# Optimization experiments

Measured on AMD Instinct MI355X. Metric: run time of the kernel, lower is better.

Reference implementation:

```python
import jax, jax.numpy as jnp
import numpy as np


def setup_inputs() -> dict:
    key = jax.random.key(0)
    k1, k2 = jax.random.split(key)
    enc = jax.random.normal(k1, (32, 64, 64, 64), dtype=jnp.float32)   # (B, C, H, W), C == D
    embed = jax.random.normal(k2, (512, 64), dtype=jnp.float32)        # (K, D) codebook
    return {"enc": enc, "embed": embed}


def reference(enc, embed):
    B, C, H, W = enc.shape
    K, D = embed.shape
    # torch: enc.view(B, -1, C) with C == D -> plain reshape (no transpose), faithful to source.
    x = enc.reshape(B, -1, D)                                          # (B, N, D), N = C*H*W/D
    # Squared L2 distances; argmin is invariant under sqrt so we skip torch.cdist's sqrt.
    x_sq = jnp.sum(x * x, axis=-1, keepdims=True)                      # (B, N, 1)
    e_sq = jnp.sum(embed * embed, axis=-1)                             # (K,)
    d2 = x_sq - 2.0 * jnp.einsum('bnd,kd->bnk', x, embed) + e_sq       # (B, N, K)
    closest = jnp.argmin(d2, axis=-1)                                  # (B, N) int
    quantized = embed[closest]                                         # (B, N, D) gather
    commitment_loss = jnp.mean((jax.lax.stop_gradient(quantized) - x) ** 2)
    codebook_loss = jnp.mean((quantized - jax.lax.stop_gradient(x)) ** 2)
    quantize_loss = codebook_loss + 1.0 * commitment_loss
    # Straight-through estimator.
    quant_out = (x + jax.lax.stop_gradient(quantized - x)).reshape(B, C, H, W)
    return quant_out, quantize_loss, closest
```

## Files before the change

kernel.cpp:

```cpp
#include <hip/hip_runtime.h>
#include <math.h>

#define DQ 64
#define KQ 512
#define NVEC 131072
#define QOUT_SIZE (NVEC * DQ)
#define LOSS_OFF QOUT_SIZE
#define IDX_OFF (QOUT_SIZE + 1)

#define RPW 32
#define WPB 4
#define VPB (RPW * WPB)
#define NBLK (NVEC / VPB)
#define SC 64
#define NST (KQ / SC)
#define SDQ (SC * DQ)
#define TIE_THR 0.01f

typedef __attribute__((ext_vector_type(8))) short short8;
typedef __attribute__((ext_vector_type(4))) float f32x4;

static __device__ __forceinline__ unsigned short f2bf(float f) {
    unsigned u = __float_as_uint(f);
    u += 0x7fff + ((u >> 16) & 1);
    return (unsigned short)(u >> 16);
}
static __device__ __forceinline__ float bf2f(unsigned short h) {
    return __uint_as_float(((unsigned)h) << 16);
}
static __device__ __forceinline__ void cvt8(float4 a, float4 b, short8& hi, short8& lo) {
#define C1(I, V) { unsigned short _h = f2bf(V); hi[I] = (short)_h; lo[I] = (short)f2bf((V) - bf2f(_h)); }
    C1(0, a.x) C1(1, a.y) C1(2, a.z) C1(3, a.w)
    C1(4, b.x) C1(5, b.y) C1(6, b.z) C1(7, b.w)
#undef C1
}

__global__ void vq_init_kernel(const float* __restrict__ embed,
                               unsigned short* __restrict__ ehi,
                               unsigned short* __restrict__ elo,
                               float* __restrict__ esq,
                               float* __restrict__ out) {
    const int t = blockIdx.x * 64 + threadIdx.x;
    if (t == 0) out[LOSS_OFF] = 0.0f;
    const int k = t >> 3;
    const int c = t & 7;
    const float4* p = (const float4*)(embed + (size_t)k * DQ + c * 8);
    float4 a = p[0], b = p[1];
    short8 hi, lo;
    cvt8(a, b, hi, lo);
    const int slot = c ^ (k & 7);
    *(short8*)(ehi + (size_t)k * DQ + slot * 8) = hi;
    *(short8*)(elo + (size_t)k * DQ + slot * 8) = lo;

    float ps = 0.f;
    ps = fmaf(a.x, a.x, ps); ps = fmaf(a.y, a.y, ps); ps = fmaf(a.z, a.z, ps); ps = fmaf(a.w, a.w, ps);
    ps = fmaf(b.x, b.x, ps); ps = fmaf(b.y, b.y, ps); ps = fmaf(b.z, b.z, ps); ps = fmaf(b.w, b.w, ps);
    ps += __shfl_xor(ps, 1);
    ps += __shfl_xor(ps, 2);
    ps += __shfl_xor(ps, 4);
    if (c == 0) esq[k] = ps;
}

__global__ __launch_bounds__(256) void vq_mfma_kernel(const float* __restrict__ enc,
                                                      const float* __restrict__ embed,
                                                      const unsigned short* __restrict__ ehi,
                                                      const unsigned short* __restrict__ elo,
                                                      const float* __restrict__ esq,
                                                      float* __restrict__ out) {
    __shared__ unsigned short hs[2 * SDQ];
    __shared__ unsigned short ls_[2 * SDQ];
    __shared__ float esq_s[KQ];
    __shared__ int bidx_s[VPB];
    __shared__ int flag_s[VPB];
    __shared__ float red[WPB];

    const int tid = threadIdx.x;
    const int lane = tid & 63;
    const int w = tid >> 6;
    const int l15 = lane & 15;
    const int l4 = lane >> 4;
    const int vb = blockIdx.x * VPB + w * RPW;

    esq_s[tid] = esq[tid];
    esq_s[tid + 256] = esq[tid + 256];

    short8 ahA[2], alA[2], ahB[2], alB[2];
#pragma unroll
    for (int a = 0; a < 2; a++) {
        const float* base = enc + (size_t)(vb + a * 16 + l15) * DQ + l4 * 8;
        const float4* p0 = (const float4*)base;
        const float4* p1 = (const float4*)(base + 32);
        cvt8(p0[0], p0[1], ahA[a], alA[a]);
        cvt8(p1[0], p1[1], ahB[a], alB[a]);
    }

    float m1[8], m2[8];
    int i1[8];
#pragma unroll
    for (int r = 0; r < 8; r++) { m1[r] = 3.4e38f; m2[r] = 3.4e38f; i1[r] = 0; }

    const int sl0 = (l4 ^ (l15 & 7)) * 8;
    const int sl1 = sl0 ^ 32;

    short8 rh0 = *(const short8*)(ehi + tid * 8);
    short8 rh1 = *(const short8*)(ehi + 2048 + tid * 8);
    short8 rl0 = *(const short8*)(elo + tid * 8);
    short8 rl1 = *(const short8*)(elo + 2048 + tid * 8);
    *(short8*)(hs + tid * 8) = rh0;  *(short8*)(hs + 2048 + tid * 8) = rh1;
    *(short8*)(ls_ + tid * 8) = rl0; *(short8*)(ls_ + 2048 + tid * 8) = rl1;
    rh0 = *(const short8*)(ehi + SDQ + tid * 8);
    rh1 = *(const short8*)(ehi + SDQ + 2048 + tid * 8);
    rl0 = *(const short8*)(elo + SDQ + tid * 8);
    rl1 = *(const short8*)(elo + SDQ + 2048 + tid * 8);

#define LDB(H0, H1, L0, L1, S) { const int _o = ((S) * 16 + l15) * DQ; \
    H0 = *(const short8*)(hb + _o + sl0); H1 = *(const short8*)(hb + _o + sl1); \
    L0 = *(const short8*)(lb + _o + sl0); L1 = *(const short8*)(lb + _o + sl1); }

#define BODY(ST, S, BH0, BH1, BL0, BL1) { \
    const int code = (ST) * SC + (S) * 16 + l15; \
    const float ev = esq_s[code]; \
    _Pragma("unroll") \
    for (int a = 0; a < 2; a++) { \
        f32x4 acc = {0.f, 0.f, 0.f, 0.f}; \
        acc = __builtin_amdgcn_mfma_f32_16x16x32_bf16(ahA[a], BH0, acc, 0, 0, 0); \
        acc = __builtin_amdgcn_mfma_f32_16x16x32_bf16(ahB[a], BH1, acc, 0, 0, 0); \
        acc = __builtin_amdgcn_mfma_f32_16x16x32_bf16(alA[a], BH0, acc, 0, 0, 0); \
        acc = __builtin_amdgcn_mfma_f32_16x16x32_bf16(alB[a], BH1, acc, 0, 0, 0); \
        acc = __builtin_amdgcn_mfma_f32_16x16x32_bf16(ahA[a], BL0, acc, 0, 0, 0); \
        acc = __builtin_amdgcn_mfma_f32_16x16x32_bf16(ahB[a], BL1, acc, 0, 0, 0); \
        _Pragma("unroll") \
        for (int r = 0; r < 4; r++) { \
            float v = fmaf(-2.0f, acc[r], ev); \
            bool lt = v < m1[a * 4 + r]; \
            i1[a * 4 + r] = lt ? code : i1[a * 4 + r]; \
            m2[a * 4 + r] = fminf(m2[a * 4 + r], fmaxf(m1[a * 4 + r], v)); \
            m1[a * 4 + r] = fminf(m1[a * 4 + r], v); \
        } \
    } }

    for (int st = 0; st < NST; st++) {
        __syncthreads();
        if (st < NST - 1) {
            unsigned short* hw = hs + ((st + 1) & 1) * SDQ;
            unsigned short* lw = ls_ + ((st + 1) & 1) * SDQ;
            *(short8*)(hw + tid * 8) = rh0;  *(short8*)(hw + 2048 + tid * 8) = rh1;
            *(short8*)(lw + tid * 8) = rl0;  *(short8*)(lw + 2048 + tid * 8) = rl1;
        }
        if (st < NST - 2) {
            const int o = (st + 2) * SDQ;
            rh0 = *(const short8*)(ehi + o + tid * 8);
            rh1 = *(const short8*)(ehi + o + 2048 + tid * 8);
            rl0 = *(const short8*)(elo + o + tid * 8);
            rl1 = *(const short8*)(elo + o + 2048 + tid * 8);
        }
        const unsigned short* hb = hs + (st & 1) * SDQ;
        const unsigned short* lb = ls_ + (st & 1) * SDQ;
        short8 b0h0, b0h1, b0l0, b0l1, b1h0, b1h1, b1l0, b1l1;
        LDB(b0h0, b0h1, b0l0, b0l1, 0)
        LDB(b1h0, b1h1, b1l0, b1l1, 1)
        BODY(st, 0, b0h0, b0h1, b0l0, b0l1)
        LDB(b0h0, b0h1, b0l0, b0l1, 2)
        BODY(st, 1, b1h0, b1h1, b1l0, b1l1)
        LDB(b1h0, b1h1, b1l0, b1l1, 3)
        BODY(st, 2, b0h0, b0h1, b0l0, b0l1)
        BODY(st, 3, b1h0, b1h1, b1l0, b1l1)
    }
#undef LDB
#undef BODY

#pragma unroll
    for (int m = 1; m <= 8; m <<= 1) {
#pragma unroll
        for (int r = 0; r < 8; r++) {
            float o1 = __shfl_xor(m1[r], m);
            float o2 = __shfl_xor(m2[r], m);
            int oi = __shfl_xor(i1[r], m);
            float nm2 = fminf(fminf(m2[r], o2), fmaxf(m1[r], o1));
            bool lt = o1 < m1[r];
            i1[r] = lt ? oi : i1[r];
            m1[r] = fminf(m1[r], o1);
            m2[r] = nm2;
        }
    }

    if (l15 == 0) {
#pragma unroll
        for (int a = 0; a < 2; a++)
#pragma unroll
            for (int r = 0; r < 4; r++) {
                const int row = a * 16 + l4 * 4 + r;
                bidx_s[w * RPW + row] = i1[a * 4 + r];
                flag_s[w * RPW + row] = (m2[a * 4 + r] - m1[a * 4 + r] < TIE_THR) ? 1 : 0;
            }
    }

    for (int row = 0; row < RPW; row++) {
        if (flag_s[w * RPW + row]) {
            const int v = vb + row;
            const float4* xe = (const float4*)(enc + (size_t)v * DQ);
            unsigned long long best = ~0ULL;
            for (int q = 0; q < 8; q++) {
                const int c = lane * 8 + q;
                const float4* ee = (const float4*)(embed + (size_t)c * DQ);
                double a = 0.0;
                for (int j = 0; j < 16; j++) {
                    float4 xx = xe[j], ez = ee[j];
                    double d0 = (double)xx.x - (double)ez.x; a = fma(d0, d0, a);
                    double d1 = (double)xx.y - (double)ez.y; a = fma(d1, d1, a);
                    double d2 = (double)xx.z - (double)ez.z; a = fma(d2, d2, a);
                    double d3 = (double)xx.w - (double)ez.w; a = fma(d3, d3, a);
                }
                unsigned long long p =
                    (((unsigned long long)__double_as_longlong(a)) & ~511ULL) | (unsigned)c;
                best = (p < best) ? p : best;
            }
#pragma unroll
            for (int mm = 1; mm < 64; mm <<= 1) {
                unsigned long long ob = (unsigned long long)__shfl_xor((long long)best, mm);
                best = (ob < best) ? ob : best;
            }
            if (lane == 0) bidx_s[w * RPW + row] = (int)(best & 511ULL);
        }
    }

    float lsum = 0.f;
#pragma unroll
    for (int a = 0; a < 2; a++) {
        const int myv = vb + a * 16 + l15;
        const int qb = bidx_s[w * RPW + a * 16 + l15];
        const float* qbase = embed + (size_t)qb * DQ + l4 * 8;
        const float4* qa = (const float4*)qbase;
        const float4* qc = (const float4*)(qbase + 32);
        float4 q0 = qa[0], q1 = qa[1], q2 = qc[0], q3 = qc[1];
        float* obase = out + (size_t)myv * DQ + l4 * 8;
        ((float4*)obase)[0] = q0; ((float4*)obase)[1] = q1;
        ((float4*)(obase + 32))[0] = q2; ((float4*)(obase + 32))[1] = q3;
        if (l4 == 0) out[IDX_OFF + myv] = (float)qb;

        float d;
        d = q0.x - (bf2f(ahA[a][0]) + bf2f(alA[a][0])); lsum = fmaf(d, d, lsum);
        d = q0.y - (bf2f(ahA[a][1]) + bf2f(alA[a][1])); lsum = fmaf(d, d, lsum);
        d = q0.z - (bf2f(ahA[a][2]) + bf2f(alA[a][2])); lsum = fmaf(d, d, lsum);
        d = q0.w - (bf2f(ahA[a][3]) + bf2f(alA[a][3])); lsum = fmaf(d, d, lsum);
        d = q1.x - (bf2f(ahA[a][4]) + bf2f(alA[a][4])); lsum = fmaf(d, d, lsum);
        d = q1.y - (bf2f(ahA[a][5]) + bf2f(alA[a][5])); lsum = fmaf(d, d, lsum);
        d = q1.z - (bf2f(ahA[a][6]) + bf2f(alA[a][6])); lsum = fmaf(d, d, lsum);
        d = q1.w - (bf2f(ahA[a][7]) + bf2f(alA[a][7])); lsum = fmaf(d, d, lsum);
        d = q2.x - (bf2f(ahB[a][0]) + bf2f(alB[a][0])); lsum = fmaf(d, d, lsum);
        d = q2.y - (bf2f(ahB[a][1]) + bf2f(alB[a][1])); lsum = fmaf(d, d, lsum);
        d = q2.z - (bf2f(ahB[a][2]) + bf2f(alB[a][2])); lsum = fmaf(d, d, lsum);
        d = q2.w - (bf2f(ahB[a][3]) + bf2f(alB[a][3])); lsum = fmaf(d, d, lsum);
        d = q3.x - (bf2f(ahB[a][4]) + bf2f(alB[a][4])); lsum = fmaf(d, d, lsum);
        d = q3.y - (bf2f(ahB[a][5]) + bf2f(alB[a][5])); lsum = fmaf(d, d, lsum);
        d = q3.z - (bf2f(ahB[a][6]) + bf2f(alB[a][6])); lsum = fmaf(d, d, lsum);
        d = q3.w - (bf2f(ahB[a][7]) + bf2f(alB[a][7])); lsum = fmaf(d, d, lsum);
    }

#pragma unroll
    for (int off = 32; off > 0; off >>= 1) lsum += __shfl_down(lsum, off);
    if (lane == 0) red[w] = lsum;
    __syncthreads();
    if (tid == 0) {
        float s = (red[0] + red[1]) + (red[2] + red[3]);
        atomicAdd(out + LOSS_OFF, s * (2.0f / (float)QOUT_SIZE));
    }
}

extern "C" void kernel_launch(void* const* d_in, const int* in_sizes, int n_in,
                              void* d_out, int out_size, void* d_ws, size_t ws_size,
                              hipStream_t stream) {
    const float* enc = (const float*)d_in[0];
    const float* embed = (const float*)d_in[1];
    float* out = (float*)d_out;
    unsigned short* ehi = (unsigned short*)d_ws;
    unsigned short* elo = ehi + KQ * DQ;
    float* esq = (float*)(elo + KQ * DQ);

    hipLaunchKernelGGL(vq_init_kernel, dim3(64), dim3(64), 0, stream,
                       embed, ehi, elo, esq, out);
    hipLaunchKernelGGL(vq_mfma_kernel, dim3(NBLK), dim3(256), 0, stream,
                       enc, embed, ehi, elo, esq, out);
}
```

Baseline: 141.7 us.

## Replace split-bf16 three-pass MFMA with single fp16 MFMA and halve block size

Measured after the change: 162.9 us. +15.0%, slower.

```diff
diff --git a/kernel.cpp b/kernel.cpp
--- a/kernel.cpp
+++ b/kernel.cpp
@@ -9,35 +9,24 @@
 #define IDX_OFF (QOUT_SIZE + 1)
 
 #define RPW 32
-#define WPB 4
+#define WPB 2
 #define VPB (RPW * WPB)
 #define NBLK (NVEC / VPB)
 #define SC 64
 #define NST (KQ / SC)
 #define SDQ (SC * DQ)
-#define TIE_THR 0.01f
-
-typedef __attribute__((ext_vector_type(8))) short short8;
+#define TIE_THR 0.05f
+
+typedef __attribute__((ext_vector_type(8))) _Float16 half8;
 typedef __attribute__((ext_vector_type(4))) float f32x4;
 
-static __device__ __forceinline__ unsigned short f2bf(float f) {
-    unsigned u = __float_as_uint(f);
-    u += 0x7fff + ((u >> 16) & 1);
-    return (unsigned short)(u >> 16);
-}
-static __device__ __forceinline__ float bf2f(unsigned short h) {
-    return __uint_as_float(((unsigned)h) << 16);
-}
-static __device__ __forceinline__ void cvt8(float4 a, float4 b, short8& hi, short8& lo) {
-#define C1(I, V) { unsigned short _h = f2bf(V); hi[I] = (short)_h; lo[I] = (short)f2bf((V) - bf2f(_h)); }
-    C1(0, a.x) C1(1, a.y) C1(2, a.z) C1(3, a.w)
-    C1(4, b.x) C1(5, b.y) C1(6, b.z) C1(7, b.w)
-#undef C1
+static __device__ __forceinline__ void cvt8h(float4 a, float4 b, half8& h) {
+    h[0] = (_Float16)a.x; h[1] = (_Float16)a.y; h[2] = (_Float16)a.z; h[3] = (_Float16)a.w;
+    h[4] = (_Float16)b.x; h[5] = (_Float16)b.y; h[6] = (_Float16)b.z; h[7] = (_Float16)b.w;
 }
 
 __global__ void vq_init_kernel(const float* __restrict__ embed,
-                               unsigned short* __restrict__ ehi,
-                               unsigned short* __restrict__ elo,
+                               unsigned short* __restrict__ eh,
                                float* __restrict__ esq,
                                float* __restrict__ out) {
     const int t = blockIdx.x * 64 + threadIdx.x;
@@ -46,11 +35,10 @@
     const int c = t & 7;
     const float4* p = (const float4*)(embed + (size_t)k * DQ + c * 8);
     float4 a = p[0], b = p[1];
-    short8 hi, lo;
-    cvt8(a, b, hi, lo);
+    half8 h;
+    cvt8h(a, b, h);
     const int slot = c ^ (k & 7);
-    *(short8*)(ehi + (size_t)k * DQ + slot * 8) = hi;
-    *(short8*)(elo + (size_t)k * DQ + slot * 8) = lo;
+    *(half8*)(eh + (size_t)k * DQ + slot * 8) = h;
 
     float ps = 0.f;
     ps = fmaf(a.x, a.x, ps); ps = fmaf(a.y, a.y, ps); ps = fmaf(a.z, a.z, ps); ps = fmaf(a.w, a.w, ps);
@@ -61,14 +49,12 @@
     if (c == 0) esq[k] = ps;
 }
 
-__global__ __launch_bounds__(256) void vq_mfma_kernel(const float* __restrict__ enc,
+__global__ __launch_bounds__(128) void vq_mfma_kernel(const float* __restrict__ enc,
                                                       const float* __restrict__ embed,
-                                                      const unsigned short* __restrict__ ehi,
-                                                      const unsigned short* __restrict__ elo,
+                                                      const unsigned short* __restrict__ eh,
                                                       const float* __restrict__ esq,
                                                       float* __restrict__ out) {
     __shared__ unsigned short hs[2 * SDQ];
-    __shared__ unsigned short ls_[2 * SDQ];
     __shared__ float esq_s[KQ];
     __shared__ int bidx_s[VPB];
     __shared__ int flag_s[VPB];
@@ -81,17 +67,19 @@
     const int l4 = lane >> 4;
     const int vb = blockIdx.x * VPB + w * RPW;
 
-    esq_s[tid] = esq[tid];
+    esq_s[tid]       = esq[tid];
+    esq_s[tid + 128] = esq[tid + 128];
     esq_s[tid + 256] = esq[tid + 256];
-
-    short8 ahA[2], alA[2], ahB[2], alB[2];
+    esq_s[tid + 384] = esq[tid + 384];
+
+    half8 ahA[2], ahB[2];
 #pragma unroll
     for (int a = 0; a < 2; a++) {
         const float* base = enc + (size_t)(vb + a * 16 + l15) * DQ + l4 * 8;
         const float4* p0 = (const float4*)base;
         const float4* p1 = (const float4*)(base + 32);
-        cvt8(p0[0], p0[1], ahA[a], alA[a]);
-        cvt8(p1[0], p1[1], ahB[a], alB[a]);
+        cvt8h(p0[0], p0[1], ahA[a]);
+        cvt8h(p1[0], p1[1], ahB[a]);
     }
 
     float m1[8], m2[8];
@@ -102,33 +90,28 @@
     const int sl0 = (l4 ^ (l15 & 7)) * 8;
     const int sl1 = sl0 ^ 32;
 
-    short8 rh0 = *(const short8*)(ehi + tid * 8);
-    short8 rh1 = *(const short8*)(ehi + 2048 + tid * 8);
-    short8 rl0 = *(const short8*)(elo + tid * 8);
-    short8 rl1 = *(const short8*)(elo + 2048 + tid * 8);
-    *(short8*)(hs + tid * 8) = rh0;  *(short8*)(hs + 2048 + tid * 8) = rh1;
-    *(short8*)(ls_ + tid * 8) = rl0; *(short8*)(ls_ + 2048 + tid * 8) = rl1;
-    rh0 = *(const short8*)(ehi + SDQ + tid * 8);
-    rh1 = *(const short8*)(ehi + SDQ + 2048 + tid * 8);
-    rl0 = *(const short8*)(elo + SDQ + tid * 8);
-    rl1 = *(const short8*)(elo + SDQ + 2048 + tid * 8);
-
-#define LDB(H0, H1, L0, L1, S) { const int _o = ((S) * 16 + l15) * DQ; \
-    H0 = *(const short8*)(hb + _o + sl0); H1 = *(const short8*)(hb + _o + sl1); \
-    L0 = *(const short8*)(lb + _o + sl0); L1 = *(const short8*)(lb + _o + sl1); }
-
-#define BODY(ST, S, BH0, BH1, BL0, BL1) { \
+    half8 r0 = *(const half8*)(eh + tid * 8);
+    half8 r1 = *(const half8*)(eh + 1024 + tid * 8);
+    half8 r2 = *(const half8*)(eh + 2048 + tid * 8);
+    half8 r3 = *(const half8*)(eh + 3072 + tid * 8);
+    *(half8*)(hs + tid * 8) = r0;        *(half8*)(hs + 1024 + tid * 8) = r1;
+    *(half8*)(hs + 2048 + tid * 8) = r2; *(half8*)(hs + 3072 + tid * 8) = r3;
+    r0 = *(const half8*)(eh + SDQ + tid * 8);
+    r1 = *(const half8*)(eh + SDQ + 1024 + tid * 8);
+    r2 = *(const half8*)(eh + SDQ + 2048 + tid * 8);
+    r3 = *(const half8*)(eh + SDQ + 3072 + tid * 8);
+
+#define LDB(B0, B1, S) { const int _o = ((S) * 16 + l15) * DQ; \
+    B0 = *(const half8*)(hb + _o + sl0); B1 = *(const half8*)(hb + _o + sl1); }
+
+#define BODY(ST, S, B0, B1) { \
     const int code = (ST) * SC + (S) * 16 + l15; \
     const float ev = esq_s[code]; \
     _Pragma("unroll") \
     for (int a = 0; a < 2; a++) { \
         f32x4 acc = {0.f, 0.f, 0.f, 0.f}; \
-        acc = __builtin_amdgcn_mfma_f32_16x16x32_bf16(ahA[a], BH0, acc, 0, 0, 0); \
-        acc = __builtin_amdgcn_mfma_f32_16x16x32_bf16(ahB[a], BH1, acc, 0, 0, 0); \
-        acc = __builtin_amdgcn_mfma_f32_16x16x32_bf16(alA[a], BH0, acc, 0, 0, 0); \
-        acc = __builtin_amdgcn_mfma_f32_16x16x32_bf16(alB[a], BH1, acc, 0, 0, 0); \
-        acc = __builtin_amdgcn_mfma_f32_16x16x32_bf16(ahA[a], BL0, acc, 0, 0, 0); \
-        acc = __builtin_amdgcn_mfma_f32_16x16x32_bf16(ahB[a], BL1, acc, 0, 0, 0); \
+        acc = __builtin_amdgcn_mfma_f32_16x16x32_f16(ahA[a], B0, acc, 0, 0, 0); \
+        acc = __builtin_amdgcn_mfma_f32_16x16x32_f16(ahB[a], B1, acc, 0, 0, 0); \
         _Pragma("unroll") \
         for (int r = 0; r < 4; r++) { \
             float v = fmaf(-2.0f, acc[r], ev); \
@@ -143,28 +126,26 @@
         __syncthreads();
         if (st < NST - 1) {
             unsigned short* hw = hs + ((st + 1) & 1) * SDQ;
-            unsigned short* lw = ls_ + ((st + 1) & 1) * SDQ;
-            *(short8*)(hw + tid * 8) = rh0;  *(short8*)(hw + 2048 + tid * 8) = rh1;
-            *(short8*)(lw + tid * 8) = rl0;  *(short8*)(lw + 2048 + tid * 8) = rl1;
+            *(half8*)(hw + tid * 8) = r0;        *(half8*)(hw + 1024 + tid * 8) = r1;
+            *(half8*)(hw + 2048 + tid * 8) = r2; *(half8*)(hw + 3072 + tid * 8) = r3;
         }
         if (st < NST - 2) {
             const int o = (st + 2) * SDQ;
-            rh0 = *(const short8*)(ehi + o + tid * 8);
-            rh1 = *(const short8*)(ehi + o + 2048 + tid * 8);
-            rl0 = *(const short8*)(elo + o + tid * 8);
-            rl1 = *(const short8*)(elo + o + 2048 + tid * 8);
+            r0 = *(const half8*)(eh + o + tid * 8);
+            r1 = *(const half8*)(eh + o + 1024 + tid * 8);
+            r2 = *(const half8*)(eh + o + 2048 + tid * 8);
+            r3 = *(const half8*)(eh + o + 3072 + tid * 8);
         }
         const unsigned short* hb = hs + (st & 1) * SDQ;
-        const unsigned short* lb = ls_ + (st & 1) * SDQ;
-        short8 b0h0, b0h1, b0l0, b0l1, b1h0, b1h1, b1l0, b1l1;
-        LDB(b0h0, b0h1, b0l0, b0l1, 0)
-        LDB(b1h0, b1h1, b1l0, b1l1, 1)
-        BODY(st, 0, b0h0, b0h1, b0l0, b0l1)
-        LDB(b0h0, b0h1, b0l0, b0l1, 2)
-        BODY(st, 1, b1h0, b1h1, b1l0, b1l1)
-        LDB(b1h0, b1h1, b1l0, b1l1, 3)
-        BODY(st, 2, b0h0, b0h1, b0l0, b0l1)
-        BODY(st, 3, b1h0, b1h1, b1l0, b1l1)
+        half8 b0h0, b0h1, b1h0, b1h1;
+        LDB(b0h0, b0h1, 0)
+        LDB(b1h0, b1h1, 1)
+        BODY(st, 0, b0h0, b0h1)
+        LDB(b0h0, b0h1, 2)
+        BODY(st, 1, b1h0, b1h1)
+        LDB(b1h0, b1h1, 3)
+        BODY(st, 2, b0h0, b0h1)
+        BODY(st, 3, b1h0, b1h1)
     }
 #undef LDB
 #undef BODY
@@ -239,22 +220,22 @@
         if (l4 == 0) out[IDX_OFF + myv] = (float)qb;
 
         float d;
-        d = q0.x - (bf2f(ahA[a][0]) + bf2f(alA[a][0])); lsum = fmaf(d, d, lsum);
-        d = q0.y - (bf2f(ahA[a][1]) + bf2f(alA[a][1])); lsum = fmaf(d, d, lsum);
-        d = q0.z - (bf2f(ahA[a][2]) + bf2f(alA[a][2])); lsum = fmaf(d, d, lsum);
-        d = q0.w - (bf2f(ahA[a][3]) + bf2f(alA[a][3])); lsum = fmaf(d, d, lsum);
-        d = q1.x - (bf2f(ahA[a][4]) + bf2f(alA[a][4])); lsum = fmaf(d, d, lsum);
-        d = q1.y - (bf2f(ahA[a][5]) + bf2f(alA[a][5])); lsum = fmaf(d, d, lsum);
-        d = q1.z - (bf2f(ahA[a][6]) + bf2f(alA[a][6])); lsum = fmaf(d, d, lsum);
-        d = q1.w - (bf2f(ahA[a][7]) + bf2f(alA[a][7])); lsum = fmaf(d, d, lsum);
-        d = q2.x - (bf2f(ahB[a][0]) + bf2f(alB[a][0])); lsum = fmaf(d, d, lsum);
-        d = q2.y - (bf2f(ahB[a][1]) + bf2f(alB[a][1])); lsum = fmaf(d, d, lsum);
-        d = q2.z - (bf2f(ahB[a][2]) + bf2f(alB[a][2])); lsum = fmaf(d, d, lsum);
-        d = q2.w - (bf2f(ahB[a][3]) + bf2f(alB[a][3])); lsum = fmaf(d, d, lsum);
-        d = q3.x - (bf2f(ahB[a][4]) + bf2f(alB[a][4])); lsum = fmaf(d, d, lsum);
-        d = q3.y - (bf2f(ahB[a][5]) + bf2f(alB[a][5])); lsum = fmaf(d, d, lsum);
-        d = q3.z - (bf2f(ahB[a][6]) + bf2f(alB[a][6])); lsum = fmaf(d, d, lsum);
-        d = q3.w - (bf2f(ahB[a][7]) + bf2f(alB[a][7])); lsum = fmaf(d, d, lsum);
+        d = q0.x - (float)ahA[a][0]; lsum = fmaf(d, d, lsum);
+        d = q0.y - (float)ahA[a][1]; lsum = fmaf(d, d, lsum);
+        d = q0.z - (float)ahA[a][2]; lsum = fmaf(d, d, lsum);
+        d = q0.w - (float)ahA[a][3]; lsum = fmaf(d, d, lsum);
+        d = q1.x - (float)ahA[a][4]; lsum = fmaf(d, d, lsum);
+        d = q1.y - (float)ahA[a][5]; lsum = fmaf(d, d, lsum);
+        d = q1.z - (float)ahA[a][6]; lsum = fmaf(d, d, lsum);
+        d = q1.w - (float)ahA[a][7]; lsum = fmaf(d, d, lsum);
+        d = q2.x - (float)ahB[a][0]; lsum = fmaf(d, d, lsum);
+        d = q2.y - (float)ahB[a][1]; lsum = fmaf(d, d, lsum);
+        d = q2.z - (float)ahB[a][2]; lsum = fmaf(d, d, lsum);
+        d = q2.w - (float)ahB[a][3]; lsum = fmaf(d, d, lsum);
+        d = q3.x - (float)ahB[a][4]; lsum = fmaf(d, d, lsum);
+        d = q3.y - (float)ahB[a][5]; lsum = fmaf(d, d, lsum);
+        d = q3.z - (float)ahB[a][6]; lsum = fmaf(d, d, lsum);
+        d = q3.w - (float)ahB[a][7]; lsum = fmaf(d, d, lsum);
     }
 
 #pragma unroll
@@ -262,7 +243,7 @@
     if (lane == 0) red[w] = lsum;
     __syncthreads();
     if (tid == 0) {
-        float s = (red[0] + red[1]) + (red[2] + red[3]);
+        float s = red[0] + red[1];
         atomicAdd(out + LOSS_OFF, s * (2.0f / (float)QOUT_SIZE));
     }
 }
@@ -273,12 +254,11 @@
     const float* enc = (const float*)d_in[0];
     const float* embed = (const float*)d_in[1];
     float* out = (float*)d_out;
-    unsigned short* ehi = (unsigned short*)d_ws;
-    unsigned short* elo = ehi + KQ * DQ;
-    float* esq = (float*)(elo + KQ * DQ);
+    unsigned short* eh = (unsigned short*)d_ws;
+    float* esq = (float*)(eh + KQ * DQ);
 
     hipLaunchKernelGGL(vq_init_kernel, dim3(64), dim3(64), 0, stream,
-                       embed, ehi, elo, esq, out);
-    hipLaunchKernelGGL(vq_mfma_kernel, dim3(NBLK), dim3(256), 0, stream,
-                       enc, embed, ehi, elo, esq, out);
-}
+                       embed, eh, esq, out);
+    hipLaunchKernelGGL(vq_mfma_kernel, dim3(NBLK), dim3(128), 0, stream,
+                       enc, embed, eh, esq, out);
+}
```
